# Kernel tuning notes

Hardware: AMD Instinct MI355X
Metric: run time of the kernel (lower is better)

## Reference

```python
import jax, jax.numpy as jnp
import numpy as np

LN_EPS = 1e-5


def setup_inputs() -> dict:
    key = jax.random.key(0)
    ks = jax.random.split(key, 6)
    B, S, D = 4, 4096, 2048
    Db = D // 4  # bottleneck_dim = n_embd // compression_ratio
    hidden = jax.random.normal(ks[0], (B, S, D), dtype=jnp.float32)
    # LayerNorm params (torch defaults: gamma=1, beta=0)
    ln_gamma = jnp.ones((D,), dtype=jnp.float32)
    ln_beta = jnp.zeros((D,), dtype=jnp.float32)
    # Linear weights, torch default init: U(-1/sqrt(fan_in), 1/sqrt(fan_in))
    bd_lim = 1.0 / np.sqrt(D)
    W_down = jax.random.uniform(ks[1], (D, Db), minval=-bd_lim, maxval=bd_lim, dtype=jnp.float32)
    b_down = jax.random.uniform(ks[2], (Db,), minval=-bd_lim, maxval=bd_lim, dtype=jnp.float32)
    bu_lim = 1.0 / np.sqrt(Db)
    W_up = jax.random.uniform(ks[3], (Db, D), minval=-bu_lim, maxval=bu_lim, dtype=jnp.float32)
    b_up = jax.random.uniform(ks[4], (D,), minval=-bu_lim, maxval=bu_lim, dtype=jnp.float32)
    alpha = jnp.array(0.01, dtype=jnp.float32)
    return {
        "hidden": hidden,
        "ln_gamma": ln_gamma,
        "ln_beta": ln_beta,
        "W_down": W_down,
        "b_down": b_down,
        "W_up": W_up,
        "b_up": b_up,
        "alpha": alpha,
        "layer_idx": 0,
    }


def reference(hidden, ln_gamma, ln_beta, W_down, b_down, W_up, b_up, alpha, layer_idx):
    # LayerNorm over last dim
    mu = jnp.mean(hidden, axis=-1, keepdims=True)
    var = jnp.mean(jnp.square(hidden - mu), axis=-1, keepdims=True)
    h_norm = (hidden - mu) * jax.lax.rsqrt(var + LN_EPS) * ln_gamma + ln_beta
    # down-proj -> SiLU -> up-proj   [b s d] @ [d k] -> [b s k] -> [b s d]
    z = jnp.einsum("bsd,dk->bsk", h_norm, W_down) + b_down
    z = jax.nn.silu(z)
    bottleneck_out = jnp.einsum("bsk,kd->bsd", z, W_up) + b_up
    # alpha-gated residual
    return hidden + alpha * (bottleneck_out - hidden)
```

## Files before the change

### kernel.cpp

```cpp
#include <hip/hip_runtime.h>

typedef __bf16 bf16x8 __attribute__((ext_vector_type(8)));
typedef __bf16 bf16x4 __attribute__((ext_vector_type(4)));
typedef float f32x4 __attribute__((ext_vector_type(4)));

#define S_BARRIER() asm volatile("s_barrier" ::: "memory")
#define WAITCNT_VM(n) asm volatile("s_waitcnt vmcnt(" #n ")" ::: "memory")
#define WAITCNT_LGKM0() asm volatile("s_waitcnt lgkmcnt(0)" ::: "memory")

__global__ __launch_bounds__(256) void prep_ln_kernel(
    const float* __restrict__ Wd, __bf16* __restrict__ Wtd,
    const float* __restrict__ Wu, __bf16* __restrict__ Wtu,
    const float* __restrict__ x, const float* __restrict__ g,
    const float* __restrict__ be, __bf16* __restrict__ y,
    int D, int Db, int ntiles) {
    if ((int)blockIdx.x < ntiles) {
        const float* W;
        __bf16* Wt;
        int K, N, tile;
        const int ntile_d = (Db / 32) * (D / 32);
        if ((int)blockIdx.x < ntile_d) {
            W = Wd; Wt = Wtd; K = D; N = Db; tile = blockIdx.x;
        } else {
            W = Wu; Wt = Wtu; K = Db; N = D; tile = blockIdx.x - ntile_d;
        }
        const int tn = tile % (N / 32), tk = tile / (N / 32);
        const int n0 = tn * 32, k0 = tk * 32;
        __shared__ float t[32][33];
        const int c = threadIdx.x & 31, r0 = threadIdx.x >> 5;
#pragma unroll
        for (int r = r0; r < 32; r += 8)
            t[r][c] = W[(size_t)(k0 + r) * N + n0 + c];
        __syncthreads();
#pragma unroll
        for (int r = r0; r < 32; r += 8)
            Wt[(size_t)(n0 + r) * K + k0 + c] = (__bf16)t[c][r];
        return;
    }
    const int t = threadIdx.x;
    const size_t row = blockIdx.x - ntiles;
    const float4* xr = (const float4*)(x + row * (size_t)D);
    const int nv = D >> 3;
    float s = 0.f, ss = 0.f;
    for (int i = t; i < nv; i += 256) {
        float4 v0 = xr[i * 2], v1 = xr[i * 2 + 1];
        s += v0.x + v0.y + v0.z + v0.w + v1.x + v1.y + v1.z + v1.w;
        ss += v0.x * v0.x + v0.y * v0.y + v0.z * v0.z + v0.w * v0.w +
              v1.x * v1.x + v1.y * v1.y + v1.z * v1.z + v1.w * v1.w;
    }
    for (int o = 32; o > 0; o >>= 1) {
        s += __shfl_down(s, o);
        ss += __shfl_down(ss, o);
    }
    __shared__ float ps[4], pss[4], mv[2];
    int w = t >> 6;
    if ((t & 63) == 0) { ps[w] = s; pss[w] = ss; }
    __syncthreads();
    if (t == 0) {
        float S = ps[0] + ps[1] + ps[2] + ps[3];
        float SS = pss[0] + pss[1] + pss[2] + pss[3];
        float mu = S / (float)D;
        float var = SS / (float)D - mu * mu;
        mv[0] = mu;
        mv[1] = rsqrtf(var + 1e-5f);
    }
    __syncthreads();
    float mu = mv[0], rstd = mv[1];
    const float4* gg = (const float4*)g;
    const float4* bb = (const float4*)be;
    bf16x8* yr = (bf16x8*)(y + row * (size_t)D);
    for (int i = t; i < nv; i += 256) {
        float4 v0 = xr[i * 2], v1 = xr[i * 2 + 1];
        float4 g0 = gg[i * 2], g1 = gg[i * 2 + 1];
        float4 b0 = bb[i * 2], b1 = bb[i * 2 + 1];
        bf16x8 o;
        o[0] = (__bf16)((v0.x - mu) * rstd * g0.x + b0.x);
        o[1] = (__bf16)((v0.y - mu) * rstd * g0.y + b0.y);
        o[2] = (__bf16)((v0.z - mu) * rstd * g0.z + b0.z);
        o[3] = (__bf16)((v0.w - mu) * rstd * g0.w + b0.w);
        o[4] = (__bf16)((v1.x - mu) * rstd * g1.x + b1.x);
        o[5] = (__bf16)((v1.y - mu) * rstd * g1.y + b1.y);
        o[6] = (__bf16)((v1.z - mu) * rstd * g1.z + b1.z);
        o[7] = (__bf16)((v1.w - mu) * rstd * g1.w + b1.w);
        yr[i] = o;
    }
}

template <int EPI>
__global__ __launch_bounds__(256, 4) void gemm_bt(const __bf16* __restrict__ A,
                                                  const __bf16* __restrict__ Bt,
                                                  const float* __restrict__ bias,
                                                  const float* __restrict__ hid,
                                                  const float* __restrict__ alpha_p,
                                                  void* __restrict__ Cout,
                                                  int M, int N, int K) {
    constexpr int BM = 128, BN = 128, BK = 32;
    __shared__ __align__(16) __bf16 Ads[2][BM * BK];
    __shared__ __align__(16) __bf16 Bds[2][BN * BK];

    const int tid = threadIdx.x;
    const int wave = tid >> 6;
    const int lane = tid & 63;
    const int bn = blockIdx.x, bm = blockIdx.y;
    const int row0 = bm * BM, col0 = bn * BN;
    const int wr = wave >> 1, wc = wave & 1;

    f32x4 acc[4][4] = {};

    const __bf16* Ag = A + (size_t)row0 * K;
    const __bf16* Bg = Bt + (size_t)col0 * K;
    const int lrow = lane >> 2;
    const int lk = ((lane & 3) ^ (lrow & 3)) * 8;

    const int c = lane & 15;
    const int q = lane >> 4;

    auto stage = [&](int k0, int b) {
#pragma unroll
        for (int p = 0; p < 2; ++p) {
            const int r = wave * 32 + p * 16;
            __builtin_amdgcn_global_load_lds(
                (__attribute__((address_space(1))) void*)(Ag + (size_t)(r + lrow) * K + k0 + lk),
                (__attribute__((address_space(3))) void*)(&Ads[b][r * BK]),
                16, 0, 0);
            __builtin_amdgcn_global_load_lds(
                (__attribute__((address_space(1))) void*)(Bg + (size_t)(r + lrow) * K + k0 + lk),
                (__attribute__((address_space(3))) void*)(&Bds[b][r * BK]),
                16, 0, 0);
        }
    };

    const int nk = K / BK;
    stage(0, 0);
    for (int it = 0; it < nk; ++it) {
        const int cur = it & 1;
        if (it + 1 < nk) {
            stage((it + 1) * BK, cur ^ 1);
            WAITCNT_VM(4);
        } else {
            WAITCNT_VM(0);
        }
        S_BARRIER();

        bf16x8 afW[4], bfA[4];
#pragma unroll
        for (int j = 0; j < 4; ++j) {
            const int rl = wc * 64 + j * 16 + c;
            afW[j] = *(const bf16x8*)(&Bds[cur][rl * BK + ((q ^ (c & 3)) * 8)]);
        }
#pragma unroll
        for (int i = 0; i < 4; ++i) {
            const int rl = wr * 64 + i * 16 + c;
            bfA[i] = *(const bf16x8*)(&Ads[cur][rl * BK + ((q ^ (c & 3)) * 8)]);
        }
#pragma unroll
        for (int i = 0; i < 4; ++i)
#pragma unroll
            for (int j = 0; j < 4; ++j)
                acc[i][j] = __builtin_amdgcn_mfma_f32_16x16x32_bf16(afW[j], bfA[i],
                                                                    acc[i][j], 0, 0, 0);
        WAITCNT_LGKM0();
        S_BARRIER();
    }

    float alpha = (EPI == 1) ? *alpha_p : 0.f;
#pragma unroll
    for (int i = 0; i < 4; ++i) {
        const int rowg = row0 + wr * 64 + i * 16 + c;
#pragma unroll
        for (int j = 0; j < 4; ++j) {
            const int colb = col0 + wc * 64 + j * 16 + q * 4;
            const float4 bv = *(const float4*)(bias + colb);
            float v0 = acc[i][j][0] + bv.x;
            float v1 = acc[i][j][1] + bv.y;
            float v2 = acc[i][j][2] + bv.z;
            float v3 = acc[i][j][3] + bv.w;
            const size_t idx = (size_t)rowg * N + colb;
            if (EPI == 0) {
                bf16x4 o;
                o[0] = (__bf16)(v0 / (1.f + __expf(-v0)));
                o[1] = (__bf16)(v1 / (1.f + __expf(-v1)));
                o[2] = (__bf16)(v2 / (1.f + __expf(-v2)));
                o[3] = (__bf16)(v3 / (1.f + __expf(-v3)));
                *(bf16x4*)((__bf16*)Cout + idx) = o;
            } else {
                const float4 h = *(const float4*)(hid + idx);
                float4 o;
                o.x = h.x + alpha * (v0 - h.x);
                o.y = h.y + alpha * (v1 - h.y);
                o.z = h.z + alpha * (v2 - h.z);
                o.w = h.w + alpha * (v3 - h.w);
                *(float4*)((float*)Cout + idx) = o;
            }
        }
    }
}

extern "C" void kernel_launch(void* const* d_in, const int* in_sizes, int n_in,
                              void* d_out, int out_size, void* d_ws, size_t ws_size,
                              hipStream_t stream) {
    const float* hidden = (const float*)d_in[0];
    const float* ln_gamma = (const float*)d_in[1];
    const float* ln_beta = (const float*)d_in[2];
    const float* W_down = (const float*)d_in[3];
    const float* b_down = (const float*)d_in[4];
    const float* W_up = (const float*)d_in[5];
    const float* b_up = (const float*)d_in[6];
    const float* alpha = (const float*)d_in[7];
    float* out = (float*)d_out;

    const int D = in_sizes[2];
    const int Db = in_sizes[4];
    const int M = in_sizes[0] / D;

    char* w = (char*)d_ws;
    __bf16* hn = (__bf16*)w;  w += (size_t)M * D * sizeof(__bf16);
    __bf16* z = (__bf16*)w;   w += (size_t)M * Db * sizeof(__bf16);
    __bf16* Wtd = (__bf16*)w; w += (size_t)D * Db * sizeof(__bf16);
    __bf16* Wtu = (__bf16*)w; w += (size_t)Db * D * sizeof(__bf16);

    const int ntiles = 2 * (D / 32) * (Db / 32);
    prep_ln_kernel<<<ntiles + M, 256, 0, stream>>>(W_down, Wtd, W_up, Wtu,
                                                   hidden, ln_gamma, ln_beta, hn,
                                                   D, Db, ntiles);

    gemm_bt<0><<<dim3(Db / 128, M / 128), 256, 0, stream>>>(
        hn, Wtd, b_down, nullptr, nullptr, (void*)z, M, Db, D);

    gemm_bt<1><<<dim3(D / 128, M / 128), 256, 0, stream>>>(
        z, Wtu, b_up, hidden, alpha, (void*)out, M, D, Db);
}
```

Measured before the change: 394.0 us.

## Triple-buffer GEMM K pipeline, shrink down-proj tile, per-wave LayerNorm rows

The GEMM now uses three LDS buffers with a prefetch distance of two and a single barrier per K step, replacing double buffering with two barriers. The down-projection runs with BM=64 tiles, which doubles its block count, since N=512 gives only 4 column tiles. The LayerNorm part assigns one row per wave and reduces with xor shuffles, so it no longer needs shared memory or __syncthreads. The costs are higher LDS use per block, which can lower occupancy, and more redundant B loads for the smaller tiles.

```diff
diff --git a/kernel.cpp b/kernel.cpp
--- a/kernel.cpp
+++ b/kernel.cpp
@@ -38,38 +38,28 @@
         return;
     }
     const int t = threadIdx.x;
-    const size_t row = blockIdx.x - ntiles;
+    const int wv = t >> 6, ln = t & 63;
+    const size_t row = (size_t)(blockIdx.x - ntiles) * 4 + wv;
     const float4* xr = (const float4*)(x + row * (size_t)D);
     const int nv = D >> 3;
     float s = 0.f, ss = 0.f;
-    for (int i = t; i < nv; i += 256) {
+    for (int i = ln; i < nv; i += 64) {
         float4 v0 = xr[i * 2], v1 = xr[i * 2 + 1];
         s += v0.x + v0.y + v0.z + v0.w + v1.x + v1.y + v1.z + v1.w;
         ss += v0.x * v0.x + v0.y * v0.y + v0.z * v0.z + v0.w * v0.w +
               v1.x * v1.x + v1.y * v1.y + v1.z * v1.z + v1.w * v1.w;
     }
+#pragma unroll
     for (int o = 32; o > 0; o >>= 1) {
-        s += __shfl_down(s, o);
-        ss += __shfl_down(ss, o);
-    }
-    __shared__ float ps[4], pss[4], mv[2];
-    int w = t >> 6;
-    if ((t & 63) == 0) { ps[w] = s; pss[w] = ss; }
-    __syncthreads();
-    if (t == 0) {
-        float S = ps[0] + ps[1] + ps[2] + ps[3];
-        float SS = pss[0] + pss[1] + pss[2] + pss[3];
-        float mu = S / (float)D;
-        float var = SS / (float)D - mu * mu;
-        mv[0] = mu;
-        mv[1] = rsqrtf(var + 1e-5f);
-    }
-    __syncthreads();
-    float mu = mv[0], rstd = mv[1];
+        s += __shfl_xor(s, o);
+        ss += __shfl_xor(ss, o);
+    }
+    const float mu = s / (float)D;
+    const float rstd = rsqrtf(ss / (float)D - mu * mu + 1e-5f);
     const float4* gg = (const float4*)g;
     const float4* bb = (const float4*)be;
     bf16x8* yr = (bf16x8*)(y + row * (size_t)D);
-    for (int i = t; i < nv; i += 256) {
+    for (int i = ln; i < nv; i += 64) {
         float4 v0 = xr[i * 2], v1 = xr[i * 2 + 1];
         float4 g0 = gg[i * 2], g1 = gg[i * 2 + 1];
         float4 b0 = bb[i * 2], b1 = bb[i * 2 + 1];
@@ -86,7 +76,7 @@
     }
 }
 
-template <int EPI>
+template <int EPI, int BM>
 __global__ __launch_bounds__(256, 4) void gemm_bt(const __bf16* __restrict__ A,
                                                   const __bf16* __restrict__ Bt,
                                                   const float* __restrict__ bias,
@@ -94,9 +84,12 @@
                                                   const float* __restrict__ alpha_p,
                                                   void* __restrict__ Cout,
                                                   int M, int N, int K) {
-    constexpr int BM = 128, BN = 128, BK = 32;
-    __shared__ __align__(16) __bf16 Ads[2][BM * BK];
-    __shared__ __align__(16) __bf16 Bds[2][BN * BK];
+    constexpr int BN = 128, BK = 32;
+    constexpr int WM = BM / 2;
+    constexpr int MI = WM / 16;
+    constexpr int GA = BM / 64;
+    __shared__ __align__(16) __bf16 Ads[3][BM * BK];
+    __shared__ __align__(16) __bf16 Bds[3][BN * BK];
 
     const int tid = threadIdx.x;
     const int wave = tid >> 6;
@@ -105,7 +98,7 @@
     const int row0 = bm * BM, col0 = bn * BN;
     const int wr = wave >> 1, wc = wave & 1;
 
-    f32x4 acc[4][4] = {};
+    f32x4 acc[MI][4] = {};
 
     const __bf16* Ag = A + (size_t)row0 * K;
     const __bf16* Bg = Bt + (size_t)col0 * K;
@@ -117,12 +110,16 @@
 
     auto stage = [&](int k0, int b) {
 #pragma unroll
-        for (int p = 0; p < 2; ++p) {
-            const int r = wave * 32 + p * 16;
+        for (int p = 0; p < GA; ++p) {
+            const int r = wave * (16 * GA) + p * 16;
             __builtin_amdgcn_global_load_lds(
                 (__attribute__((address_space(1))) void*)(Ag + (size_t)(r + lrow) * K + k0 + lk),
                 (__attribute__((address_space(3))) void*)(&Ads[b][r * BK]),
                 16, 0, 0);
+        }
+#pragma unroll
+        for (int p = 0; p < 2; ++p) {
+            const int r = wave * 32 + p * 16;
             __builtin_amdgcn_global_load_lds(
                 (__attribute__((address_space(1))) void*)(Bg + (size_t)(r + lrow) * K + k0 + lk),
                 (__attribute__((address_space(3))) void*)(&Bds[b][r * BK]),
@@ -132,41 +129,43 @@
 
     const int nk = K / BK;
     stage(0, 0);
+    if (nk > 1) stage(BK, 1);
+    int cur = 0, pf = 2;
     for (int it = 0; it < nk; ++it) {
-        const int cur = it & 1;
         if (it + 1 < nk) {
-            stage((it + 1) * BK, cur ^ 1);
-            WAITCNT_VM(4);
+            if constexpr (GA == 2) WAITCNT_VM(4); else WAITCNT_VM(3);
         } else {
             WAITCNT_VM(0);
         }
+        WAITCNT_LGKM0();
         S_BARRIER();
-
-        bf16x8 afW[4], bfA[4];
+        if (it + 2 < nk) stage((it + 2) * BK, pf);
+
+        bf16x8 afW[4], bfA[MI];
 #pragma unroll
         for (int j = 0; j < 4; ++j) {
             const int rl = wc * 64 + j * 16 + c;
             afW[j] = *(const bf16x8*)(&Bds[cur][rl * BK + ((q ^ (c & 3)) * 8)]);
         }
 #pragma unroll
-        for (int i = 0; i < 4; ++i) {
-            const int rl = wr * 64 + i * 16 + c;
+        for (int i = 0; i < MI; ++i) {
+            const int rl = wr * WM + i * 16 + c;
             bfA[i] = *(const bf16x8*)(&Ads[cur][rl * BK + ((q ^ (c & 3)) * 8)]);
         }
 #pragma unroll
-        for (int i = 0; i < 4; ++i)
+        for (int i = 0; i < MI; ++i)
 #pragma unroll
             for (int j = 0; j < 4; ++j)
                 acc[i][j] = __builtin_amdgcn_mfma_f32_16x16x32_bf16(afW[j], bfA[i],
                                                                     acc[i][j], 0, 0, 0);
-        WAITCNT_LGKM0();
-        S_BARRIER();
+        cur = (cur + 1 == 3) ? 0 : cur + 1;
+        pf = (pf + 1 == 3) ? 0 : pf + 1;
     }
 
     float alpha = (EPI == 1) ? *alpha_p : 0.f;
 #pragma unroll
-    for (int i = 0; i < 4; ++i) {
-        const int rowg = row0 + wr * 64 + i * 16 + c;
+    for (int i = 0; i < MI; ++i) {
+        const int rowg = row0 + wr * WM + i * 16 + c;
 #pragma unroll
         for (int j = 0; j < 4; ++j) {
             const int colb = col0 + wc * 64 + j * 16 + q * 4;
@@ -220,13 +219,13 @@
     __bf16* Wtu = (__bf16*)w; w += (size_t)Db * D * sizeof(__bf16);
 
     const int ntiles = 2 * (D / 32) * (Db / 32);
-    prep_ln_kernel<<<ntiles + M, 256, 0, stream>>>(W_down, Wtd, W_up, Wtu,
-                                                   hidden, ln_gamma, ln_beta, hn,
-                                                   D, Db, ntiles);
-
-    gemm_bt<0><<<dim3(Db / 128, M / 128), 256, 0, stream>>>(
+    prep_ln_kernel<<<ntiles + M / 4, 256, 0, stream>>>(W_down, Wtd, W_up, Wtu,
+                                                       hidden, ln_gamma, ln_beta, hn,
+                                                       D, Db, ntiles);
+
+    gemm_bt<0, 64><<<dim3(Db / 128, M / 64), 256, 0, stream>>>(
         hn, Wtd, b_down, nullptr, nullptr, (void*)z, M, Db, D);
 
-    gemm_bt<1><<<dim3(D / 128, M / 128), 256, 0, stream>>>(
+    gemm_bt<1, 128><<<dim3(D / 128, M / 128), 256, 0, stream>>>(
         z, Wtu, b_up, hidden, alpha, (void*)out, M, D, Db);
 }
```

Result: no change. 400.7 us (+1.7%).
